# Kernel optimization log

Measured on AMD Instinct MI355X. Metric: run time of the kernel, lower is better.

The kernel has to match this reference:

```python
import jax, jax.numpy as jnp
import numpy as np

BATCH, SEQ, IN_DIM, UNITS = 64, 512, 512, 512


def setup_inputs() -> dict:
    key = jax.random.key(0)
    k1, k2, k3 = jax.random.split(key, 3)
    # Glorot-uniform-ish init for input kernel, orthogonal-like (normal) for recurrent
    lim = (6.0 / (IN_DIM + UNITS)) ** 0.5
    x = jax.random.normal(k1, (BATCH, SEQ, IN_DIM), dtype=jnp.float32)
    W_in = jax.random.uniform(k2, (IN_DIM, UNITS), dtype=jnp.float32, minval=-lim, maxval=lim)
    W_rec = jax.random.normal(k3, (UNITS, UNITS), dtype=jnp.float32) / (UNITS ** 0.5)
    b = jnp.zeros((UNITS,), dtype=jnp.float32)
    return {"x": x, "W_in": W_in, "W_rec": W_rec, "b": b}


def reference(x, W_in, W_rec, b):
    # SimpleRNN: h_t = tanh(x_t @ W_in + h_{t-1} @ W_rec + b), return all h_t.
    # Precompute the input projection for all timesteps in one big GEMM,
    # then scan only the small recurrent matmul + tanh.
    xw = jnp.einsum('bti,iu->btu', x, W_in) + b  # [B,T,U]
    xw_t = jnp.swapaxes(xw, 0, 1)                # [T,B,U] for scan over time

    def step(h, xw_step):
        h_new = jnp.tanh(xw_step + h @ W_rec)
        return h_new, h_new

    h0 = jnp.zeros((x.shape[0], W_rec.shape[0]), dtype=x.dtype)
    _, hs = jax.lax.scan(step, h0, xw_t)         # hs: [T,B,U]
    return jnp.swapaxes(hs, 0, 1)                # [B,T,U]
```

## Files before the change

### kernel.cpp

```cpp
#include <hip/hip_runtime.h>
#include <hip/hip_bf16.h>
#include <math.h>


#define B_ 64
#define T_ 512
#define U_ 512

__global__ __launch_bounds__(256)
void rnn_inproj_gemm(const float* __restrict__ X, const float* __restrict__ Win,
                     const float* __restrict__ bias, float* __restrict__ out) {
    __shared__ float As[16][128];
    __shared__ float Bs[16][128];

    const int m0 = blockIdx.x * 128;
    const int n0 = blockIdx.y * 128;
    const int tid = threadIdx.x;
    const int tx = tid & 15;
    const int ty = tid >> 4;

    float acc[8][8];
#pragma unroll
    for (int i = 0; i < 8; ++i)
#pragma unroll
        for (int j = 0; j < 8; ++j) acc[i][j] = 0.f;

    for (int k0 = 0; k0 < 512; k0 += 16) {
#pragma unroll
        for (int i = 0; i < 2; ++i) {
            int li = tid * 2 + i;
            int row = li >> 2;
            int c4 = li & 3;
            float4 v = *(const float4*)&X[(size_t)(m0 + row) * 512 + k0 + c4 * 4];
            As[c4 * 4 + 0][row] = v.x;
            As[c4 * 4 + 1][row] = v.y;
            As[c4 * 4 + 2][row] = v.z;
            As[c4 * 4 + 3][row] = v.w;
        }
#pragma unroll
        for (int i = 0; i < 2; ++i) {
            int li = tid * 2 + i;
            int row = li >> 5;
            int c4 = li & 31;
            float4 v = *(const float4*)&Win[(size_t)(k0 + row) * 512 + n0 + c4 * 4];
            *(float4*)&Bs[row][c4 * 4] = v;
        }
        __syncthreads();

#pragma unroll
        for (int k = 0; k < 16; ++k) {
            float a[8], b[8];
            *(float4*)&a[0] = *(float4*)&As[k][ty * 8];
            *(float4*)&a[4] = *(float4*)&As[k][ty * 8 + 4];
            *(float4*)&b[0] = *(float4*)&Bs[k][tx * 8];
            *(float4*)&b[4] = *(float4*)&Bs[k][tx * 8 + 4];
#pragma unroll
            for (int i = 0; i < 8; ++i)
#pragma unroll
                for (int j = 0; j < 8; ++j) acc[i][j] += a[i] * b[j];
        }
        __syncthreads();
    }

#pragma unroll
    for (int i = 0; i < 8; ++i) {
        int m = m0 + ty * 8 + i;
#pragma unroll
        for (int j = 0; j < 8; j += 4) {
            int n = n0 + tx * 8 + j;
            float4 bv = *(const float4*)&bias[n];
            float4 o;
            o.x = acc[i][j + 0] + bv.x;
            o.y = acc[i][j + 1] + bv.y;
            o.z = acc[i][j + 2] + bv.z;
            o.w = acc[i][j + 3] + bv.w;
            *(float4*)&out[(size_t)m * 512 + n] = o;
        }
    }
}


__device__ __forceinline__ float lane_bcast(float v, int l) {
    return __int_as_float(__builtin_amdgcn_readlane(__float_as_int(v), l));
}

__global__ __launch_bounds__(512, 1)
void rnn_scan(const float* __restrict__ Wrec, float* __restrict__ out,
              unsigned* __restrict__ cnt) {
    __shared__ float Wl[512][64];
    __shared__ float part[4][2][64];

    const int bid = blockIdx.x;
    const int xcd = bid & 7;
    const int r = bid >> 3;
    const int slot = r >> 3;
    const int j = r & 7;
    const int g = xcd + 8 * slot;

    const int u0 = j * 64;
    const int tid = threadIdx.x;
    const int lane = tid & 63;
    const int w = tid >> 6;
    const int ks = w >> 1;
    const int b = w & 1;
    const int bb = 2 * g + b;

    for (int i = tid; i < 512 * 16; i += 512) {
        int k = i >> 4;
        int c4 = i & 15;
        float4 v = *(const float4*)&Wrec[(size_t)k * 512 + u0 + c4 * 4];
        *(float4*)&Wl[k][c4 * 4] = v;
    }
    __syncthreads();

    unsigned* myc = cnt + g * 16;

    const int kb = ks * 128;
    float* const rowbase = out + (size_t)bb * T_ * U_;

    const int b2 = tid >> 6;
    const int u = tid & 63;
    float* const predptr = out + ((size_t)(2 * g + b2) * T_) * U_ + u0 + u;

    for (int t = 0; t < T_; ++t) {
        float xwv = 0.f;
        if (tid < 128) xwv = predptr[(size_t)t * U_];

        float hr0, hr1;
        if (t == 0) {
            hr0 = 0.f; hr1 = 0.f;
        } else {
            const float* hp = rowbase + (size_t)(t - 1) * U_ + kb;
            hr0 = hp[lane];
            hr1 = hp[64 + lane];
        }

        float a0 = 0.f, a1 = 0.f, a2 = 0.f, a3 = 0.f;
        if (t == 0) {
        } else {
#pragma unroll
            for (int q = 0; q < 64; q += 4) {
                a0 += lane_bcast(hr0, q + 0) * Wl[kb + q + 0][lane];
                a1 += lane_bcast(hr0, q + 1) * Wl[kb + q + 1][lane];
                a2 += lane_bcast(hr0, q + 2) * Wl[kb + q + 2][lane];
                a3 += lane_bcast(hr0, q + 3) * Wl[kb + q + 3][lane];
            }
#pragma unroll
            for (int q = 0; q < 64; q += 4) {
                a0 += lane_bcast(hr1, q + 0) * Wl[kb + 64 + q + 0][lane];
                a1 += lane_bcast(hr1, q + 1) * Wl[kb + 64 + q + 1][lane];
                a2 += lane_bcast(hr1, q + 2) * Wl[kb + 64 + q + 2][lane];
                a3 += lane_bcast(hr1, q + 3) * Wl[kb + 64 + q + 3][lane];
            }
        }
        part[ks][b][lane] = (a0 + a1) + (a2 + a3);
        __syncthreads();

        if (tid < 128) {
            float s = part[0][b2][u] + part[1][b2][u] + part[2][b2][u] + part[3][b2][u];
            predptr[(size_t)t * U_] = tanhf(xwv + s);
        }
        __syncthreads();

        if (tid == 0) {
            __threadfence();
            atomicAdd(myc, 1u);
            const unsigned target = 8u * (t + 1);
            while (__hip_atomic_load(myc, __ATOMIC_ACQUIRE, __HIP_MEMORY_SCOPE_AGENT) < target) {
                __builtin_amdgcn_s_sleep(8);
            }
        }
        __syncthreads();
    }
}

extern "C" void kernel_launch(void* const* d_in, const int* in_sizes, int n_in,
                              void* d_out, int out_size, void* d_ws, size_t ws_size,
                              hipStream_t stream) {
    const float* x    = (const float*)d_in[0];
    const float* Win  = (const float*)d_in[1];
    const float* Wrec = (const float*)d_in[2];
    const float* bias = (const float*)d_in[3];
    float* out = (float*)d_out;

    hipMemsetAsync(d_ws, 0, 2048, stream);

    dim3 gA(256, 4), bA(256);
    rnn_inproj_gemm<<<gA, bA, 0, stream>>>(x, Win, bias, out);

    unsigned* cnt = (unsigned*)d_ws;
    void* args[] = { (void*)&Wrec, (void*)&out, (void*)&cnt };
    hipLaunchCooperativeKernel((const void*)rnn_scan, dim3(256), dim3(512), args, 0, stream);
}
```

Measured before the change: 4.220 ms.

## Replace per-step group barrier with per-producer flags and wave-level waits

Replaces the atomic-counter barrier across the 8 blocks of a batch group with per-(block, batch-row) flags that each producer sets with a release store after writing its h slice. Each wave now spins only on the two producer flags it actually reads, and the partial-sum buffer is double-buffered so a block-wide sync per step can be removed. This aims to cut barrier latency and let waves proceed as soon as their inputs are ready, at the cost of more flag polling traffic and finer-grained memory-ordering reasoning.

```diff
diff --git a/kernel.cpp b/kernel.cpp
--- a/kernel.cpp
+++ b/kernel.cpp
@@ -86,9 +86,9 @@
 
 __global__ __launch_bounds__(512, 1)
 void rnn_scan(const float* __restrict__ Wrec, float* __restrict__ out,
-              unsigned* __restrict__ cnt) {
+              unsigned* __restrict__ flags) {
     __shared__ float Wl[512][64];
-    __shared__ float part[4][2][64];
+    __shared__ float part[2][4][2][64];
 
     const int bid = blockIdx.x;
     const int xcd = bid & 7;
@@ -113,31 +113,35 @@
     }
     __syncthreads();
 
-    unsigned* myc = cnt + g * 16;
-
     const int kb = ks * 128;
-    float* const rowbase = out + (size_t)bb * T_ * U_;
+    const float* const rowbase = out + (size_t)bb * T_ * U_;
 
     const int b2 = tid >> 6;
     const int u = tid & 63;
-    float* const predptr = out + ((size_t)(2 * g + b2) * T_) * U_ + u0 + u;
+    float* const hptr = out + (size_t)(2 * g + b2) * T_ * U_ + u0 + u;
+    unsigned* const myflag  = flags + g * 16 + j * 2 + b2;
+    unsigned* const srcflag = flags + g * 16 + (2 * ks + (lane & 1)) * 2 + b;
 
     for (int t = 0; t < T_; ++t) {
         float xwv = 0.f;
-        if (tid < 128) xwv = predptr[(size_t)t * U_];
+        if (tid < 128) xwv = hptr[(size_t)t * U_];
 
-        float hr0, hr1;
-        if (t == 0) {
-            hr0 = 0.f; hr1 = 0.f;
-        } else {
+        if (t > 0) {
+            const unsigned tgt = (unsigned)t;
+            bool ok;
+            do {
+                unsigned v = tgt;
+                if (lane < 2)
+                    v = __hip_atomic_load(srcflag, __ATOMIC_RELAXED, __HIP_MEMORY_SCOPE_AGENT);
+                ok = __all((int)(v >= tgt));
+            } while (!ok);
+            __builtin_amdgcn_fence(__ATOMIC_ACQUIRE, "agent");
+
             const float* hp = rowbase + (size_t)(t - 1) * U_ + kb;
-            hr0 = hp[lane];
-            hr1 = hp[64 + lane];
-        }
+            float hr0 = hp[lane];
+            float hr1 = hp[64 + lane];
 
-        float a0 = 0.f, a1 = 0.f, a2 = 0.f, a3 = 0.f;
-        if (t == 0) {
-        } else {
+            float a0 = 0.f, a1 = 0.f, a2 = 0.f, a3 = 0.f;
 #pragma unroll
             for (int q = 0; q < 64; q += 4) {
                 a0 += lane_bcast(hr0, q + 0) * Wl[kb + q + 0][lane];
@@ -152,25 +156,21 @@
                 a2 += lane_bcast(hr1, q + 2) * Wl[kb + 64 + q + 2][lane];
                 a3 += lane_bcast(hr1, q + 3) * Wl[kb + 64 + q + 3][lane];
             }
+            part[t & 1][ks][b][lane] = (a0 + a1) + (a2 + a3);
         }
-        part[ks][b][lane] = (a0 + a1) + (a2 + a3);
         __syncthreads();
 
         if (tid < 128) {
-            float s = part[0][b2][u] + part[1][b2][u] + part[2][b2][u] + part[3][b2][u];
-            predptr[(size_t)t * U_] = tanhf(xwv + s);
+            float s = 0.f;
+            if (t > 0) {
+                const float* pp = &part[t & 1][0][b2][u];
+                s = (pp[0] + pp[128]) + (pp[256] + pp[384]);
+            }
+            hptr[(size_t)t * U_] = tanhf(xwv + s);
+            if (lane == 0)
+                __hip_atomic_store(myflag, (unsigned)(t + 1), __ATOMIC_RELEASE,
+                                   __HIP_MEMORY_SCOPE_AGENT);
         }
-        __syncthreads();
-
-        if (tid == 0) {
-            __threadfence();
-            atomicAdd(myc, 1u);
-            const unsigned target = 8u * (t + 1);
-            while (__hip_atomic_load(myc, __ATOMIC_ACQUIRE, __HIP_MEMORY_SCOPE_AGENT) < target) {
-                __builtin_amdgcn_s_sleep(8);
-            }
-        }
-        __syncthreads();
     }
 }
 
@@ -188,7 +188,7 @@
     dim3 gA(256, 4), bA(256);
     rnn_inproj_gemm<<<gA, bA, 0, stream>>>(x, Win, bias, out);
 
-    unsigned* cnt = (unsigned*)d_ws;
-    void* args[] = { (void*)&Wrec, (void*)&out, (void*)&cnt };
+    unsigned* flags = (unsigned*)d_ws;
+    void* args[] = { (void*)&Wrec, (void*)&out, (void*)&flags };
     hipLaunchCooperativeKernel((const void*)rnn_scan, dim3(256), dim3(512), args, 0, stream);
 }
```

Result: slower. 10.86 ms (+157.4%).
